# Kernel optimization log

Measured on AMD Instinct MI355X. Metric: run time of the kernel, lower is better.

The kernel has to match this reference:

```python
import jax, jax.numpy as jnp
import numpy as np

N = 50000      # nodes
E = 800000     # edges (avg degree 16)
IN = 256       # in_size
HID = 64       # hid_size
H = 4          # n_head
OUT = 64       # out_size


def setup_inputs() -> dict:
    key = jax.random.key(0)
    ks = jax.random.split(key, 16)
    g = lambda k, shp: jax.random.normal(k, shp, jnp.float32) * 0.1
    return {
        "features": jax.random.normal(ks[0], (N, IN), jnp.float32),
        "src": jax.random.randint(ks[1], (E,), 0, N, jnp.int32),
        "dst": jax.random.randint(ks[2], (E,), 0, N, jnp.int32),
        # layer 0: 256 -> 4 heads x 64
        "W0": g(ks[3], (IN, H * HID)), "al0": g(ks[4], (H, HID)), "ar0": g(ks[5], (H, HID)), "b0": g(ks[6], (H * HID,)),
        # layer 1: 256 -> 4 heads x 64
        "W1": g(ks[7], (H * HID, H * HID)), "al1": g(ks[8], (H, HID)), "ar1": g(ks[9], (H, HID)), "b1": g(ks[10], (H * HID,)),
        # layer 2: 256 -> 4 heads x 64, relu activation, mean over heads
        "W2": g(ks[11], (H * HID, H * OUT)), "al2": g(ks[12], (H, OUT)), "ar2": g(ks[13], (H, OUT)), "b2": g(ks[14], (H * OUT,)),
    }


def gat_conv(h, src, dst, W, al, ar, b, apply_relu):
    """DGL GATConv (eval mode, dropout off), residual identity since in == H*D."""
    n = h.shape[0]
    hh, dd = al.shape
    feat = (h @ W).reshape(n, hh, dd)                       # [N,H,D]
    el = jnp.einsum('nhd,hd->nh', feat, al)                 # [N,H]
    er = jnp.einsum('nhd,hd->nh', feat, ar)                 # [N,H]
    e = jax.nn.leaky_relu(el[src] + er[dst], negative_slope=0.2)  # [E,H]
    # segment softmax over incoming edges of each dst node
    m = jax.ops.segment_max(e, dst, num_segments=n)         # [N,H]
    ex = jnp.exp(e - m[dst])
    den = jax.ops.segment_sum(ex, dst, num_segments=n)      # [N,H]
    alpha = ex / den[dst]                                   # [E,H]
    rst = jax.ops.segment_sum(feat[src] * alpha[..., None], dst, num_segments=n)  # [N,H,D]
    rst = rst + h.reshape(n, hh, dd) + b.reshape(1, hh, dd)  # residual + bias
    return jax.nn.relu(rst) if apply_relu else rst


def reference(features, src, dst, W0, al0, ar0, b0, W1, al1, ar1, b1, W2, al2, ar2, b2):
    h = gat_conv(features, src, dst, W0, al0, ar0, b0, False).reshape(N, -1)
    h = gat_conv(h, src, dst, W1, al1, ar1, b1, False).reshape(N, -1)
    h = gat_conv(h, src, dst, W2, al2, ar2, b2, True).mean(axis=1)  # [N,OUT]
    return h
```

## Files before the change

kernel.cpp:

```cpp
#include <hip/hip_runtime.h>

#define NNODE 50000
#define NEDGE 800000
#define NH 4
#define DH 64
#define HD 256
#define PADN 50048
#define EPAD 64

typedef __attribute__((ext_vector_type(8))) _Float16 half8v;
typedef __attribute__((ext_vector_type(2))) _Float16 half2v;
typedef __attribute__((ext_vector_type(4))) float float4v;

static __device__ __forceinline__ unsigned short f2h(float f) {
  return __builtin_bit_cast(unsigned short, (_Float16)f);
}

__global__ __launch_bounds__(256) void k_prep(const float* __restrict__ W0,
                                              const float* __restrict__ W1,
                                              const float* __restrict__ W2,
                                              const float* __restrict__ al0,
                                              const float* __restrict__ ar0,
                                              const float* __restrict__ al1,
                                              const float* __restrict__ ar1,
                                              const float* __restrict__ al2,
                                              const float* __restrict__ ar2,
                                              unsigned short* __restrict__ F0,
                                              unsigned short* __restrict__ F1,
                                              unsigned short* __restrict__ F2,
                                              unsigned short* __restrict__ G0,
                                              unsigned short* __restrict__ G1,
                                              unsigned short* __restrict__ G2) {
  int L = blockIdx.y;
  const float* W = L == 0 ? W0 : (L == 1 ? W1 : W2);
  if (blockIdx.x < 32) {
    unsigned short* F = L == 0 ? F0 : (L == 1 ? F1 : F2);
    int idx = blockIdx.x * 256 + threadIdx.x;
    int lane = idx & 63;
    int ni = (idx >> 6) & 3;
    int head = (idx >> 8) & 3;
    int t = idx >> 10;
    int row = head * 64 + ni * 16 + (lane & 15);
    int kb = t * 32 + (lane >> 4) * 8;
    unsigned short v[8];
#pragma unroll
    for (int j = 0; j < 8; ++j) v[j] = f2h(W[(size_t)(kb + j) * HD + row]);
    *(uint4*)(F + (size_t)idx * 8) = *(const uint4*)v;
  } else {
    const float* al = L == 0 ? al0 : (L == 1 ? al1 : al2);
    const float* ar = L == 0 ? ar0 : (L == 1 ? ar1 : ar2);
    unsigned short* G = L == 0 ? G0 : (L == 1 ? G1 : G2);
    int k = threadIdx.x;
    const float* wr = W + (size_t)k * HD;
    float s[8] = {};
#pragma unroll
    for (int h = 0; h < 4; ++h)
#pragma unroll 4
      for (int dq = 0; dq < 16; ++dq) {
        float4v w4 = *(const float4v*)(wr + h * 64 + dq * 4);
        const float* alp = al + h * 64 + dq * 4;
        const float* arp = ar + h * 64 + dq * 4;
#pragma unroll
        for (int j = 0; j < 4; ++j) {
          s[h] = fmaf(w4[j], alp[j], s[h]);
          s[4 + h] = fmaf(w4[j], arp[j], s[4 + h]);
        }
      }
    int base = (k >> 5) * 512 + ((k >> 3) & 3) * 128 + (k & 7);
#pragma unroll
    for (int j = 0; j < 8; ++j) G[base + j * 8] = f2h(s[j]);
#pragma unroll
    for (int j = 8; j < 16; ++j) G[base + j * 8] = 0;
  }
}

__global__ void k_edge(const int* __restrict__ src, const int* __restrict__ dst,
                       int* __restrict__ fill, int* __restrict__ csrp) {
  int e = blockIdx.x * 256 + threadIdx.x;
  if (e < NEDGE) {
    int d = dst[e];
    int pos = atomicAdd(&fill[d], 1);
    if (pos < EPAD) csrp[(d << 6) + pos] = src[e];
  }
}

template <bool FP32A>
__global__ __launch_bounds__(256) void k_gemm(const float* __restrict__ Af,
                                              const unsigned short* __restrict__ Ab,
                                              const unsigned short* __restrict__ Wtf,
                                              const unsigned short* __restrict__ walrf,
                                              unsigned short* __restrict__ featb,
                                              float* __restrict__ el,
                                              float* __restrict__ er) {
  __shared__ unsigned short As[8][32][40];
  const int row0 = blockIdx.x * 32;
  const int tid = threadIdx.x;
  const int lane = tid & 63;
  const int head = tid >> 6;
  const int lr = lane & 15;
  const int kf = (lane >> 4) * 8;

  {
    const int r = tid >> 3, c = tid & 7;
    int grow = row0 + r;
    if (FP32A) {
      int gr = grow < NNODE ? grow : 0;
      const float* ap = Af + (size_t)gr * HD;
#pragma unroll
      for (int j = 0; j < 4; ++j) {
        int col8 = c + j * 8;
        float4v f0 = *(const float4v*)(ap + col8 * 8);
        float4v f1 = *(const float4v*)(ap + col8 * 8 + 4);
        uint4 pk;
        pk.x = (unsigned)f2h(f0.x) | ((unsigned)f2h(f0.y) << 16);
        pk.y = (unsigned)f2h(f0.z) | ((unsigned)f2h(f0.w) << 16);
        pk.z = (unsigned)f2h(f1.x) | ((unsigned)f2h(f1.y) << 16);
        pk.w = (unsigned)f2h(f1.z) | ((unsigned)f2h(f1.w) << 16);
        *(uint4*)&As[col8 >> 2][r][(col8 & 3) * 8] = pk;
      }
    } else {
      const unsigned short* ap = Ab + (size_t)grow * HD;
#pragma unroll
      for (int j = 0; j < 4; ++j) {
        int col8 = c + j * 8;
        *(uint4*)&As[col8 >> 2][r][(col8 & 3) * 8] = *(const uint4*)(ap + col8 * 8);
      }
    }
  }
  __syncthreads();

  float4v acc[2][4] = {};
  float4v acc_e = {};
  const bool do_e = head < 2;

  const unsigned short* wb = Wtf + (size_t)(head * 4 * 64 + lane) * 8;
  half8v bc[4], bn[4], be, ben;
#pragma unroll
  for (int ni = 0; ni < 4; ++ni) bc[ni] = *(const half8v*)(wb + ni * 512);
  if (do_e) be = *(const half8v*)(walrf + (size_t)lane * 8);

#pragma unroll
  for (int t = 0; t < 8; ++t) {
    if (t < 7) {
#pragma unroll
      for (int ni = 0; ni < 4; ++ni)
        bn[ni] = *(const half8v*)(wb + (size_t)(t + 1) * 8192 + ni * 512);
      if (do_e) ben = *(const half8v*)(walrf + (size_t)((t + 1) * 64 + lane) * 8);
    }
    half8v af[2];
#pragma unroll
    for (int mi = 0; mi < 2; ++mi)
      af[mi] = *(const half8v*)&As[t][mi * 16 + lr][kf];
#pragma unroll
    for (int mi = 0; mi < 2; ++mi)
#pragma unroll
      for (int ni = 0; ni < 4; ++ni)
        acc[mi][ni] = __builtin_amdgcn_mfma_f32_16x16x32_f16(bc[ni], af[mi], acc[mi][ni], 0, 0, 0);
    if (do_e)
      acc_e = __builtin_amdgcn_mfma_f32_16x16x32_f16(af[head & 1], be, acc_e, 0, 0, 0);
#pragma unroll
    for (int ni = 0; ni < 4; ++ni) bc[ni] = bn[ni];
    be = ben;
  }

  const int rg = (lane >> 4) * 4;

#pragma unroll
  for (int mi = 0; mi < 2; ++mi) {
    int node = row0 + mi * 16 + lr;
    if (node < NNODE) {
#pragma unroll
      for (int ni = 0; ni < 4; ++ni) {
        uint2 o;
        o.x = (unsigned)f2h(acc[mi][ni][0]) | ((unsigned)f2h(acc[mi][ni][1]) << 16);
        o.y = (unsigned)f2h(acc[mi][ni][2]) | ((unsigned)f2h(acc[mi][ni][3]) << 16);
        *(uint2*)(featb + (size_t)node * HD + head * 64 + ni * 16 + rg) = o;
      }
    }
  }

#pragma unroll
  for (int reg = 0; reg < 4; ++reg) {
    int grow = row0 + (head & 1) * 16 + rg + reg;
    if (do_e && grow < NNODE) {
      if (lr < 4) el[grow * NH + lr] = acc_e[reg];
      else if (lr < 8) er[grow * NH + lr - 4] = acc_e[reg];
    }
  }
}

template <int LAYER>
__global__ __launch_bounds__(256) void k_agg(const int* __restrict__ fillarr,
                                             const int* __restrict__ csrp,
                                             const float* __restrict__ el,
                                             const float* __restrict__ er,
                                             const unsigned short* __restrict__ featb,
                                             const unsigned short* __restrict__ hinb,
                                             const float* __restrict__ hinf,
                                             const float* __restrict__ bias,
                                             void* __restrict__ outv) {
  const int tid = threadIdx.x;
  const int w = tid >> 6;
  const int lane = tid & 63;
  const int n = blockIdx.x * 4 + w;
  const int e2 = lane >> 5;
  const int h = (lane >> 3) & 3;
  const int dg = lane & 7;
  const int deg = min(fillarr[n], EPAD);

  __shared__ float alpha_s[4][64][4];
  __shared__ int src_s[4][64];

  const float4v er4 = *(const float4v*)(er + n * 4);

  int s = 0;
  float4v lg = {-1e30f, -1e30f, -1e30f, -1e30f};
  if (lane < deg) {
    s = csrp[(n << 6) + lane];
    float4v e4 = *(const float4v*)(el + s * 4);
#pragma unroll
    for (int c = 0; c < 4; ++c) {
      float x = e4[c] + er4[c];
      lg[c] = x > 0.f ? x : 0.2f * x;
    }
  }
  float4v p;
#pragma unroll
  for (int c = 0; c < 4; ++c) p[c] = __expf(lg[c]);
  *(float4v*)&alpha_s[w][lane][0] = p;
  src_s[w][lane] = s;

  float acc[8] = {};
  float aden = 0.f;
  const int foff = (h << 6) + (dg << 3);
  int nit = (((deg + 1) >> 1) + 3) & ~3;
  for (int pj = 0; pj < nit; pj += 4) {
    float a[4];
    int sv[4];
    uint4 u[4];
#pragma unroll
    for (int q = 0; q < 4; ++q) {
      int e = ((pj + q) << 1) + e2;
      a[q] = alpha_s[w][e][h];
      sv[q] = src_s[w][e];
    }
#pragma unroll
    for (int q = 0; q < 4; ++q)
      u[q] = *(const uint4*)(featb + ((size_t)sv[q] << 8) + foff);
#pragma unroll
    for (int q = 0; q < 4; ++q) {
      aden += a[q];
      unsigned uu[4] = {u[q].x, u[q].y, u[q].z, u[q].w};
#pragma unroll
      for (int t = 0; t < 4; ++t) {
        half2v hp = __builtin_bit_cast(half2v, uu[t]);
        acc[2 * t] = fmaf(a[q], (float)hp[0], acc[2 * t]);
        acc[2 * t + 1] = fmaf(a[q], (float)hp[1], acc[2 * t + 1]);
      }
    }
  }
#pragma unroll
  for (int k = 0; k < 8; ++k) acc[k] += __shfl_xor(acc[k], 32, 64);
  aden += __shfl_xor(aden, 32, 64);

  float inv = aden > 0.f ? 1.f / aden : 0.f;

  float hr[8];
  if (LAYER == 0) {
    const float4v* hp = (const float4v*)(hinf + ((size_t)n << 8) + foff);
    float4v h0 = hp[0], h1 = hp[1];
    hr[0] = h0.x; hr[1] = h0.y; hr[2] = h0.z; hr[3] = h0.w;
    hr[4] = h1.x; hr[5] = h1.y; hr[6] = h1.z; hr[7] = h1.w;
  } else {
    uint4 hv = *(const uint4*)(hinb + ((size_t)n << 8) + foff);
    unsigned hh[4] = {hv.x, hv.y, hv.z, hv.w};
#pragma unroll
    for (int k = 0; k < 4; ++k) {
      half2v hp = __builtin_bit_cast(half2v, hh[k]);
      hr[2 * k] = (float)hp[0];
      hr[2 * k + 1] = (float)hp[1];
    }
  }
  const float4v* bp = (const float4v*)(bias + foff);
  float4v bb0 = bp[0], bb1 = bp[1];
  float bb[8] = {bb0.x, bb0.y, bb0.z, bb0.w, bb1.x, bb1.y, bb1.z, bb1.w};
  float v[8];
#pragma unroll
  for (int k = 0; k < 8; ++k) v[k] = acc[k] * inv + hr[k] + bb[k];

  if (LAYER == 2) {
#pragma unroll
    for (int k = 0; k < 8; ++k) {
      v[k] = fmaxf(v[k], 0.f);
      v[k] += __shfl_xor(v[k], 8, 64);
      v[k] += __shfl_xor(v[k], 16, 64);
      v[k] *= 0.25f;
    }
    if (lane < 8) {
      float* out = (float*)outv + (size_t)n * DH + (dg << 3);
      *(float4v*)out = (float4v){v[0], v[1], v[2], v[3]};
      *(float4v*)(out + 4) = (float4v){v[4], v[5], v[6], v[7]};
    }
  } else {
    if (e2 == 0) {
      uint4 o;
      unsigned ov[4];
#pragma unroll
      for (int q = 0; q < 4; ++q)
        ov[q] = (unsigned)f2h(v[2 * q]) | ((unsigned)f2h(v[2 * q + 1]) << 16);
      o.x = ov[0]; o.y = ov[1]; o.z = ov[2]; o.w = ov[3];
      *(uint4*)((unsigned short*)outv + ((size_t)n << 8) + foff) = o;
    }
  }
}

extern "C" void kernel_launch(void* const* d_in, const int* in_sizes, int n_in,
                              void* d_out, int out_size, void* d_ws, size_t ws_size,
                              hipStream_t stream) {
  const float* features = (const float*)d_in[0];
  const int* src = (const int*)d_in[1];
  const int* dst = (const int*)d_in[2];
  const float* W0 = (const float*)d_in[3];
  const float* al0 = (const float*)d_in[4];
  const float* ar0 = (const float*)d_in[5];
  const float* b0 = (const float*)d_in[6];
  const float* W1 = (const float*)d_in[7];
  const float* al1 = (const float*)d_in[8];
  const float* ar1 = (const float*)d_in[9];
  const float* b1 = (const float*)d_in[10];
  const float* W2 = (const float*)d_in[11];
  const float* al2 = (const float*)d_in[12];
  const float* ar2 = (const float*)d_in[13];
  const float* b2 = (const float*)d_in[14];
  float* out = (float*)d_out;

  char* p = (char*)d_ws;
  auto carve = [&](size_t bytes) {
    char* q = p;
    p += (bytes + 255) & ~(size_t)255;
    return q;
  };
  unsigned short* h1b = (unsigned short*)carve((size_t)PADN * HD * 2);
  unsigned short* h2b = (unsigned short*)carve((size_t)PADN * HD * 2);
  unsigned short* featb = (unsigned short*)carve((size_t)PADN * HD * 2);
  unsigned short* wtf0 = (unsigned short*)carve((size_t)8192 * 8 * 2);
  unsigned short* wtf1 = (unsigned short*)carve((size_t)8192 * 8 * 2);
  unsigned short* wtf2 = (unsigned short*)carve((size_t)8192 * 8 * 2);
  unsigned short* walf0 = (unsigned short*)carve((size_t)8 * 512 * 2);
  unsigned short* walf1 = (unsigned short*)carve((size_t)8 * 512 * 2);
  unsigned short* walf2 = (unsigned short*)carve((size_t)8 * 512 * 2);
  float* el = (float*)carve((size_t)NNODE * NH * 4);
  float* er = (float*)carve((size_t)NNODE * NH * 4);
  int* fill = (int*)carve((size_t)NNODE * 4);
  int* csrp = (int*)carve((size_t)NNODE * EPAD * 4);

  hipMemsetAsync(fill, 0, (size_t)NNODE * 4, stream);

  k_prep<<<dim3(33, 3), 256, 0, stream>>>(W0, W1, W2, al0, ar0, al1, ar1, al2, ar2,
                                          wtf0, wtf1, wtf2, walf0, walf1, walf2);
  k_edge<<<NEDGE / 256, 256, 0, stream>>>(src, dst, fill, csrp);

  dim3 gg(PADN / 32);

  k_gemm<true><<<gg, 256, 0, stream>>>(features, nullptr, wtf0, walf0, featb, el, er);
  k_agg<0><<<NNODE / 4, 256, 0, stream>>>(fill, csrp, el, er, featb, nullptr, features, b0, h1b);

  k_gemm<false><<<gg, 256, 0, stream>>>(nullptr, h1b, wtf1, walf1, featb, el, er);
  k_agg<1><<<NNODE / 4, 256, 0, stream>>>(fill, csrp, el, er, featb, h1b, nullptr, b1, h2b);

  k_gemm<false><<<gg, 256, 0, stream>>>(nullptr, h2b, wtf2, walf2, featb, el, er);
  k_agg<2><<<NNODE / 4, 256, 0, stream>>>(fill, csrp, el, er, featb, h2b, nullptr, b2, (void*)out);
}
```

Measured before the change: 343.3 us.

## Fuse edge bucketing into first GEMM launch and triple-buffer weight prefetch

The standalone edge-bucketing kernel is merged into the first-layer GEMM launch as extra blocks, so CSR construction runs alongside the GEMM and one launch and its serialization point go away. The GEMM's weight fragment prefetch also changes from double to triple buffering, loading two K-steps ahead to hide more global-load latency. This adds register pressure from the extra buffers, and the atomic-heavy edge blocks now compete with GEMM blocks for compute units.

```diff
diff --git a/kernel.cpp b/kernel.cpp
--- a/kernel.cpp
+++ b/kernel.cpp
@@ -7,6 +7,8 @@
 #define HD 256
 #define PADN 50048
 #define EPAD 64
+#define GEMMB (PADN / 32)
+#define EDGEB (NEDGE / 256)
 
 typedef __attribute__((ext_vector_type(8))) _Float16 half8v;
 typedef __attribute__((ext_vector_type(2))) _Float16 half2v;
@@ -74,25 +76,28 @@
   }
 }
 
-__global__ void k_edge(const int* __restrict__ src, const int* __restrict__ dst,
-                       int* __restrict__ fill, int* __restrict__ csrp) {
-  int e = blockIdx.x * 256 + threadIdx.x;
-  if (e < NEDGE) {
-    int d = dst[e];
-    int pos = atomicAdd(&fill[d], 1);
-    if (pos < EPAD) csrp[(d << 6) + pos] = src[e];
-  }
-}
-
-template <bool FP32A>
+template <bool FP32A, bool EDGE>
 __global__ __launch_bounds__(256) void k_gemm(const float* __restrict__ Af,
                                               const unsigned short* __restrict__ Ab,
                                               const unsigned short* __restrict__ Wtf,
                                               const unsigned short* __restrict__ walrf,
                                               unsigned short* __restrict__ featb,
                                               float* __restrict__ el,
-                                              float* __restrict__ er) {
+                                              float* __restrict__ er,
+                                              const int* __restrict__ esrc,
+                                              const int* __restrict__ edst,
+                                              int* __restrict__ fill,
+                                              int* __restrict__ csrp) {
   __shared__ unsigned short As[8][32][40];
+  if (EDGE && blockIdx.x >= GEMMB) {
+    int e = (blockIdx.x - GEMMB) * 256 + threadIdx.x;
+    if (e < NEDGE) {
+      int d = edst[e];
+      int pos = atomicAdd(&fill[d], 1);
+      if (pos < EPAD) csrp[(d << 6) + pos] = esrc[e];
+    }
+    return;
+  }
   const int row0 = blockIdx.x * 32;
   const int tid = threadIdx.x;
   const int lane = tid & 63;
@@ -134,18 +139,24 @@
   const bool do_e = head < 2;
 
   const unsigned short* wb = Wtf + (size_t)(head * 4 * 64 + lane) * 8;
-  half8v bc[4], bn[4], be, ben;
-#pragma unroll
-  for (int ni = 0; ni < 4; ++ni) bc[ni] = *(const half8v*)(wb + ni * 512);
-  if (do_e) be = *(const half8v*)(walrf + (size_t)lane * 8);
+  half8v bb[3][4], beb[3];
+#pragma unroll
+  for (int ni = 0; ni < 4; ++ni) {
+    bb[0][ni] = *(const half8v*)(wb + ni * 512);
+    bb[1][ni] = *(const half8v*)(wb + 8192 + ni * 512);
+  }
+  if (do_e) {
+    beb[0] = *(const half8v*)(walrf + (size_t)lane * 8);
+    beb[1] = *(const half8v*)(walrf + (size_t)(64 + lane) * 8);
+  }
 
 #pragma unroll
   for (int t = 0; t < 8; ++t) {
-    if (t < 7) {
+    if (t < 6) {
 #pragma unroll
       for (int ni = 0; ni < 4; ++ni)
-        bn[ni] = *(const half8v*)(wb + (size_t)(t + 1) * 8192 + ni * 512);
-      if (do_e) ben = *(const half8v*)(walrf + (size_t)((t + 1) * 64 + lane) * 8);
+        bb[(t + 2) % 3][ni] = *(const half8v*)(wb + (size_t)(t + 2) * 8192 + ni * 512);
+      if (do_e) beb[(t + 2) % 3] = *(const half8v*)(walrf + (size_t)((t + 2) * 64 + lane) * 8);
     }
     half8v af[2];
 #pragma unroll
@@ -155,12 +166,9 @@
     for (int mi = 0; mi < 2; ++mi)
 #pragma unroll
       for (int ni = 0; ni < 4; ++ni)
-        acc[mi][ni] = __builtin_amdgcn_mfma_f32_16x16x32_f16(bc[ni], af[mi], acc[mi][ni], 0, 0, 0);
+        acc[mi][ni] = __builtin_amdgcn_mfma_f32_16x16x32_f16(bb[t % 3][ni], af[mi], acc[mi][ni], 0, 0, 0);
     if (do_e)
-      acc_e = __builtin_amdgcn_mfma_f32_16x16x32_f16(af[head & 1], be, acc_e, 0, 0, 0);
-#pragma unroll
-    for (int ni = 0; ni < 4; ++ni) bc[ni] = bn[ni];
-    be = ben;
+      acc_e = __builtin_amdgcn_mfma_f32_16x16x32_f16(af[head & 1], beb[t % 3], acc_e, 0, 0, 0);
   }
 
   const int rg = (lane >> 4) * 4;
@@ -358,16 +366,16 @@
 
   k_prep<<<dim3(33, 3), 256, 0, stream>>>(W0, W1, W2, al0, ar0, al1, ar1, al2, ar2,
                                           wtf0, wtf1, wtf2, walf0, walf1, walf2);
-  k_edge<<<NEDGE / 256, 256, 0, stream>>>(src, dst, fill, csrp);
-
-  dim3 gg(PADN / 32);
-
-  k_gemm<true><<<gg, 256, 0, stream>>>(features, nullptr, wtf0, walf0, featb, el, er);
+
+  k_gemm<true, true><<<GEMMB + EDGEB, 256, 0, stream>>>(
+      features, nullptr, wtf0, walf0, featb, el, er, src, dst, fill, csrp);
   k_agg<0><<<NNODE / 4, 256, 0, stream>>>(fill, csrp, el, er, featb, nullptr, features, b0, h1b);
 
-  k_gemm<false><<<gg, 256, 0, stream>>>(nullptr, h1b, wtf1, walf1, featb, el, er);
+  k_gemm<false, false><<<GEMMB, 256, 0, stream>>>(
+      nullptr, h1b, wtf1, walf1, featb, el, er, nullptr, nullptr, nullptr, nullptr);
   k_agg<1><<<NNODE / 4, 256, 0, stream>>>(fill, csrp, el, er, featb, h1b, nullptr, b1, h2b);
 
-  k_gemm<false><<<gg, 256, 0, stream>>>(nullptr, h2b, wtf2, walf2, featb, el, er);
+  k_gemm<false, false><<<GEMMB, 256, 0, stream>>>(
+      nullptr, h2b, wtf2, walf2, featb, el, er, nullptr, nullptr, nullptr, nullptr);
   k_agg<2><<<NNODE / 4, 256, 0, stream>>>(fill, csrp, el, er, featb, h2b, nullptr, b2, (void*)out);
 }
```

Result: slower. 353.9 us (+3.1%).
